# Kernel optimization log

Hardware: AMD Instinct MI355X
Metric: run time of the kernel (lower is better)

Reference implementation:

```python
import jax, jax.numpy as jnp
import numpy as np

R = 10000   # relation_num
E = 256     # emb_size == hidden_size
B = 1024    # batch
L = 8       # body length (loop runs L-1 steps)


def setup_inputs() -> dict:
    key = jax.random.key(0)
    ks = jax.random.split(key, 10)
    s = 0.05
    return {
        "bodys": jax.random.randint(ks[0], (B, L), 0, R),
        "emb_w": jax.random.normal(ks[1], (R, E), jnp.float32) * s,
        "w_ih": jax.random.normal(ks[2], (4 * E, E), jnp.float32) * s,
        "w_hh": jax.random.normal(ks[3], (4 * E, E), jnp.float32) * s,
        "b_ih": jax.random.normal(ks[4], (4 * E,), jnp.float32) * s,
        "b_hh": jax.random.normal(ks[5], (4 * E,), jnp.float32) * s,
        "fc1_w": jax.random.normal(ks[6], (E, 2 * E), jnp.float32) * s,
        "fc1_b": jax.random.normal(ks[7], (E,), jnp.float32) * s,
        "fc2_w": jax.random.normal(ks[8], (R + 1, E), jnp.float32) * s,
        "fc2_b": jax.random.normal(ks[9], (R + 1,), jnp.float32) * s,
    }


def _lstm(x, w_ih, w_hh, b_ih, b_hh):
    # x: [B, L, E] -> hidden states [B, L, H] (torch gate order i,f,g,o)
    Bn, _, H = x.shape[0], x.shape[1], w_hh.shape[1]
    h0 = jnp.zeros((Bn, H), x.dtype)
    c0 = jnp.zeros((Bn, H), x.dtype)

    def step(carry, xt):
        h, c = carry
        g = xt @ w_ih.T + b_ih + h @ w_hh.T + b_hh
        i, f, gg, o = jnp.split(g, 4, axis=-1)
        c = jax.nn.sigmoid(f) * c + jax.nn.sigmoid(i) * jnp.tanh(gg)
        h = jax.nn.sigmoid(o) * jnp.tanh(c)
        return (h, c), h

    _, hs = jax.lax.scan(step, (h0, c0), x.transpose(1, 0, 2))
    return hs.transpose(1, 0, 2)


def reference(bodys, emb_w, w_ih, w_hh, b_ih, b_hh, fc1_w, fc1_b, fc2_w, fc2_b):
    x = emb_w[bodys]                       # [B, L, E] embedded body relations
    body_hid = _lstm(x, w_ih, w_hh, b_ih, b_hh)  # [B, L, E]
    Rn = emb_w.shape[0]
    prob = emb_concat = prob_sf = None
    for i in range(body_hid.shape[1] - 1):   # short fixed unroll (L-1 steps)
        if i == 0:
            emb_1 = x[:, 0, :]
            second = x[:, 1, :]
        else:
            # prob_sf @ cat(embedding(indices), body_hid[:, i])  without [B,R+1,E]
            emb_1 = prob_sf[:, :Rn] @ emb_w + prob_sf[:, Rn:] * body_hid[:, i, :]
            # relation_emb[:, i+1, :] == emb_w[i+1] broadcast over batch
            second = jnp.broadcast_to(emb_w[i + 1], emb_1.shape)
        emb_concat = jnp.concatenate([emb_1, second], axis=1)   # [B, 2E]
        prob = jax.nn.relu(emb_concat @ fc1_w.T + fc1_b) @ fc2_w.T + fc2_b  # [B, R+1]
        prob_sf = jax.nn.softmax(prob, axis=1)
    return prob, emb_concat
```

## Files before the change

### kernel.cpp

```cpp
#include <hip/hip_runtime.h>

#define Bv 1024
#define Ev 256
#define Lv 8
#define Rv 10000
#define NP1 10001
#define PS2 10240
#define NPAD 10112
#define BM 64
#define BN 128
#define BK 32
#define NSLICE 16
#define NSLOT 158
#define RPSTRIDE 160

typedef __attribute__((ext_vector_type(8))) short bf16x8;
typedef __attribute__((ext_vector_type(4))) float f32x4;

__device__ __forceinline__ float b2f(unsigned short u) {
    union { unsigned int i; float f; } v; v.i = ((unsigned int)u) << 16; return v.f;
}
__device__ __forceinline__ unsigned short f2b(float f) {
    union { float f; unsigned int i; } v; v.f = f;
    unsigned int r = v.i + 0x7fffu + ((v.i >> 16) & 1u);
    return (unsigned short)(r >> 16);
}
__device__ __forceinline__ void glds16(const void* g, void* l) {
    __builtin_amdgcn_global_load_lds(
        (const __attribute__((address_space(1))) void*)g,
        (__attribute__((address_space(3))) void*)l, 16, 0, 0);
}

__global__ __launch_bounds__(256) void gemm_tile(
    const unsigned short* __restrict__ A1, int lda1,
    const unsigned short* __restrict__ W1, int ldw1,
    const float* __restrict__ bias1,
    int Ktot, int kchunk, int Ncols, int mode,
    float* __restrict__ outF, unsigned short* __restrict__ outB, int ldc,
    float* __restrict__ rowPart, float* __restrict__ sfLastU)
{
    __shared__ unsigned short As[BM * BK];
    __shared__ unsigned short Bs[BN * BK];

    int bmode = mode & 7;
    int swz   = mode >> 4;
    int bx, by, bz;
    if (swz == 1) {
        int r = blockIdx.x & 7, q = blockIdx.x >> 3;
        bx = q & 15; by = r + (q >> 4) * 8; bz = 0;
        if (by >= NPAD / BN) return;
    } else if (swz == 2) {
        int r = blockIdx.x & 7, q = blockIdx.x >> 3;
        bz = r + (q >> 5) * 8; bx = (q & 31) >> 1; by = q & 1;
    } else {
        bx = blockIdx.x; by = blockIdx.y; bz = blockIdx.z;
    }

    int tid  = threadIdx.x;
    int wave = tid >> 6;
    int lane = tid & 63;
    int quad = lane >> 4;
    int l16  = lane & 15;
    int wm = (wave & 1) * 32;
    int wn = (wave >> 1) * 64;
    int m0 = bx * BM;
    int n0 = by * BN;
    int k0 = bz * kchunk;
    int k1 = k0 + kchunk; if (k1 > Ktot) k1 = Ktot;

    f32x4 acc[2][4];
#pragma unroll
    for (int i = 0; i < 2; ++i)
#pragma unroll
        for (int j = 0; j < 4; ++j) acc[i][j] = (f32x4){0.f, 0.f, 0.f, 0.f};

    int c0 = tid, c1 = 256 + tid;
    int row0 = c0 >> 2, row1 = c1 >> 2;
    int g80 = ((c0 & 3) ^ (row0 & 3) ^ ((row0 >> 2) & 3)) * 8;
    int g81 = ((c1 & 3) ^ (row1 & 3) ^ ((row1 >> 2) & 3)) * 8;
    unsigned short* ldsA0 = As + (size_t)(wave * 64) * 8;
    unsigned short* ldsB0 = Bs + (size_t)(wave * 64) * 8;
    unsigned short* ldsB1 = Bs + (size_t)(256 + wave * 64) * 8;

    bool first = true;
    for (int k = k0; k < k1; k += BK) {
        if (!first) __syncthreads();
        first = false;
        glds16(A1 + (size_t)(m0 + row0) * lda1 + k + g80, ldsA0);
        glds16(W1 + (size_t)(n0 + row0) * ldw1 + k + g80, ldsB0);
        glds16(W1 + (size_t)(n0 + row1) * ldw1 + k + g81, ldsB1);
        asm volatile("s_waitcnt vmcnt(0)" ::: "memory");
        __syncthreads();

        bf16x8 af[2], bfr[4];
#pragma unroll
        for (int t = 0; t < 2; ++t) {
            int m = wm + t * 16 + l16;
            int ca = quad ^ (m & 3) ^ ((m >> 2) & 3);
            af[t] = *(const bf16x8*)(As + m * 32 + ca * 8);
        }
#pragma unroll
        for (int t = 0; t < 4; ++t) {
            int n = wn + t * 16 + l16;
            int cb = quad ^ (n & 3) ^ ((n >> 2) & 3);
            bfr[t] = *(const bf16x8*)(Bs + n * 32 + cb * 8);
        }
#pragma unroll
        for (int i = 0; i < 2; ++i)
#pragma unroll
            for (int j = 0; j < 4; ++j)
                acc[i][j] = __builtin_amdgcn_mfma_f32_16x16x32_bf16(
                    af[i], bfr[j], acc[i][j], 0, 0, 0);
    }

    if (bmode == 5) {
        float rsum[2][4];
#pragma unroll
        for (int i = 0; i < 2; ++i)
#pragma unroll
            for (int r = 0; r < 4; ++r) rsum[i][r] = 0.f;
#pragma unroll
        for (int j = 0; j < 4; ++j) {
            int n = n0 + wn + j * 16 + l16;
            bool valid = (n < Ncols);
            float bsum = valid ? bias1[n] : 0.f;
#pragma unroll
            for (int i = 0; i < 2; ++i) {
                int mBase = m0 + wm + i * 16 + quad * 4;
#pragma unroll
                for (int r = 0; r < 4; ++r) {
                    float e = 0.f;
                    unsigned short w = 0;
                    if (valid) {
                        e = expf(acc[i][j][r] + bsum);
                        w = f2b(e);
                        if (n == Rv) sfLastU[mBase + r] = e;
                    }
                    outB[(size_t)(mBase + r) * ldc + n] = w;
                    rsum[i][r] += e;
                }
            }
        }
        int slot = by * 2 + (wn >> 6);
#pragma unroll
        for (int i = 0; i < 2; ++i)
#pragma unroll
            for (int r = 0; r < 4; ++r) {
                float s = rsum[i][r];
                s += __shfl_xor(s, 1);
                s += __shfl_xor(s, 2);
                s += __shfl_xor(s, 4);
                s += __shfl_xor(s, 8);
                if (l16 == 0) {
                    int m = m0 + wm + i * 16 + quad * 4 + r;
                    rowPart[(size_t)m * RPSTRIDE + slot] = s;
                }
            }
        return;
    }

#pragma unroll
    for (int j = 0; j < 4; ++j) {
        int n = n0 + wn + j * 16 + l16;
        if (n >= Ncols) continue;
        float bsum = bias1 ? bias1[n] : 0.f;
#pragma unroll
        for (int i = 0; i < 2; ++i) {
            int mBase = m0 + wm + i * 16 + quad * 4;
#pragma unroll
            for (int r = 0; r < 4; ++r) {
                float v = acc[i][j][r] + bsum;
                size_t idx = (size_t)(mBase + r) * ldc + n;
                if (bmode == 0)      outF[idx] = v;
                else                 outF[(size_t)bz * (Bv * Ev) + idx] = v;
            }
        }
    }
}

__global__ __launch_bounds__(256) void gemm64(
    const unsigned short* __restrict__ A1, int lda1,
    const unsigned short* __restrict__ W1, int ldw1,
    const unsigned short* __restrict__ A2, int lda2,
    const unsigned short* __restrict__ W2, int ldw2,
    const float* __restrict__ bias1,
    int Ktot, int Ncols, int mode,
    float* __restrict__ outF, unsigned short* __restrict__ outB,
    int ldc, int nshift)
{
    __shared__ unsigned short As[64 * 32];
    __shared__ unsigned short Bs[64 * 32];

    int bmode = mode & 7;
    int bx = blockIdx.x >> nshift;
    int by = blockIdx.x & ((1 << nshift) - 1);
    int tid  = threadIdx.x;
    int wave = tid >> 6;
    int lane = tid & 63;
    int quad = lane >> 4;
    int l16  = lane & 15;
    int m0 = bx * 64;
    int n0 = by * 64;

    f32x4 acc[4];
#pragma unroll
    for (int j = 0; j < 4; ++j) acc[j] = (f32x4){0.f, 0.f, 0.f, 0.f};

    int row = tid >> 2;
    int g8  = ((tid & 3) ^ (row & 3) ^ ((row >> 2) & 3)) * 8;
    unsigned short* ldsA = As + wave * 512;
    unsigned short* ldsB = Bs + wave * 512;

    int nSrc = A2 ? 2 : 1;
    bool first = true;
    for (int s = 0; s < nSrc; ++s) {
        const unsigned short* A = s ? A2 : A1; int lda = s ? lda2 : lda1;
        const unsigned short* W = s ? W2 : W1; int ldw = s ? ldw2 : ldw1;
        for (int k = 0; k < Ktot; k += 32) {
            if (!first) __syncthreads();
            first = false;
            glds16(A + (size_t)(m0 + row) * lda + k + g8, ldsA);
            glds16(W + (size_t)(n0 + row) * ldw + k + g8, ldsB);
            asm volatile("s_waitcnt vmcnt(0)" ::: "memory");
            __syncthreads();

            int ml = wave * 16 + l16;
            int ca = quad ^ (ml & 3) ^ ((ml >> 2) & 3);
            bf16x8 a = *(const bf16x8*)(As + ml * 32 + ca * 8);
#pragma unroll
            for (int j = 0; j < 4; ++j) {
                int nl = j * 16 + l16;
                int cb = quad ^ (nl & 3) ^ ((nl >> 2) & 3);
                bf16x8 b = *(const bf16x8*)(Bs + nl * 32 + cb * 8);
                acc[j] = __builtin_amdgcn_mfma_f32_16x16x32_bf16(a, b, acc[j], 0, 0, 0);
            }
        }
    }

    if (bmode == 4) {
        int e  = by * 16 + l16;
        float bi = bias1[n0 + l16];
        float bf_ = bias1[n0 + 16 + l16];
        float bg = bias1[n0 + 32 + l16];
        float bo = bias1[n0 + 48 + l16];
#pragma unroll
        for (int r = 0; r < 4; ++r) {
            int m = m0 + wave * 16 + quad * 4 + r;
            float gi = acc[0][r] + bi;
            float gf = acc[1][r] + bf_;
            float gg = acc[2][r] + bg;
            float go = acc[3][r] + bo;
            float cp = (mode & 8) ? 0.f : outF[(size_t)m * 256 + e];
            float si = 1.f / (1.f + expf(-gi));
            float sf = 1.f / (1.f + expf(-gf));
            float so = 1.f / (1.f + expf(-go));
            float cn = sf * cp + si * tanhf(gg);
            outF[(size_t)m * 256 + e] = cn;
            outB[(size_t)m * 256 + e] = f2b(so * tanhf(cn));
        }
        return;
    }

#pragma unroll
    for (int j = 0; j < 4; ++j) {
        int n = n0 + j * 16 + l16;
        if (n >= Ncols) continue;
        float bsum = bias1 ? bias1[n] : 0.f;
#pragma unroll
        for (int r = 0; r < 4; ++r) {
            int m = m0 + wave * 16 + quad * 4 + r;
            float v = acc[j][r] + bsum;
            if (bmode == 1) outB[(size_t)m * ldc + n] = f2b(v > 0.f ? v : 0.f);
            else            outB[(size_t)m * ldc + n] = f2b(v);
        }
    }
}

__global__ void prep_k(const float* __restrict__ w_ih,
                       const float* __restrict__ w_hh,
                       const float* __restrict__ fc1_w,
                       const float* __restrict__ fc2_w,
                       const float* __restrict__ b_ih,
                       const float* __restrict__ b_hh,
                       const int* __restrict__ bodys,
                       const float* __restrict__ emb_w,
                       unsigned short* __restrict__ w_ih_b,
                       unsigned short* __restrict__ w_hh_b,
                       unsigned short* __restrict__ fc1_w_b,
                       unsigned short* __restrict__ fc2_w_b,
                       float* __restrict__ biasC,
                       unsigned short* __restrict__ x)
{
    int b = blockIdx.x, t = threadIdx.x;
    if (b < 1264) {
#pragma unroll
        for (int j = 0; j < 8; ++j) {
            int i = b * 2048 + j * 256 + t;
            fc2_w_b[i] = (i < NP1 * Ev) ? f2b(fc2_w[i]) : (unsigned short)0;
        }
    } else if (b < 1520) {
        int bb = b - 1264;
        const float* src = (bb < 128) ? w_ih : w_hh;
        unsigned short* dst = (bb < 128) ? w_ih_b : w_hh_b;
        int rb = (bb & 127) * 8;
#pragma unroll
        for (int j = 0; j < 8; ++j) {
            int r = rb + j;
            int gate = (r >> 4) & 3;
            int e = (r & 15) | ((r >> 6) << 4);
            dst[(size_t)r * 256 + t] = f2b(src[(size_t)(gate * 256 + e) * 256 + t]);
        }
    } else if (b < 1584) {
        int base = (b - 1520) * 2048;
#pragma unroll
        for (int j = 0; j < 8; ++j) {
            int i = base + j * 256 + t;
            fc1_w_b[i] = f2b(fc1_w[i]);
        }
    } else if (b < 1585) {
#pragma unroll
        for (int j = 0; j < 4; ++j) {
            int r = j * 256 + t;
            int gate = (r >> 4) & 3;
            int e = (r & 15) | ((r >> 6) << 4);
            biasC[r] = b_ih[gate * 256 + e] + b_hh[gate * 256 + e];
        }
    } else {
        int bb = b - 1585;
#pragma unroll
        for (int j = 0; j < 8; ++j) {
            int row = bb * 8 + j;
            x[(size_t)row * Ev + t] = f2b(emb_w[(size_t)bodys[row] * Ev + t]);
        }
    }
}

__global__ void transpose_emb(const float* __restrict__ emb_w,
                              unsigned short* __restrict__ embT)
{
    __shared__ float tile[32][33];
    int kt = blockIdx.x * 32, et = blockIdx.y * 32;
    int tx = threadIdx.x & 31, ty = threadIdx.x >> 5;
#pragma unroll
    for (int r = ty; r < 32; r += 8) {
        int k = kt + r;
        tile[r][tx] = (k < Rv) ? emb_w[(size_t)k * Ev + et + tx] : 0.f;
    }
    __syncthreads();
#pragma unroll
    for (int r = ty; r < 32; r += 8) {
        embT[(size_t)(et + r) * PS2 + kt + tx] = f2b(tile[tx][r]);
    }
}

__global__ void concat0(const int* __restrict__ bodys,
                        const float* __restrict__ emb_w,
                        unsigned short* __restrict__ embc,
                        unsigned short* __restrict__ sfA)
{
    int b = blockIdx.x, e = threadIdx.x;
    embc[(size_t)b * 512 + e]       = f2b(emb_w[(size_t)bodys[b * Lv + 0] * Ev + e]);
    embc[(size_t)b * 512 + 256 + e] = f2b(emb_w[(size_t)bodys[b * Lv + 1] * Ev + e]);
    if (e < PS2 - NPAD) sfA[(size_t)b * PS2 + NPAD + e] = 0;
}

__global__ void finalize_emb(const float* __restrict__ emb1p,
                             const float* __restrict__ rowPart,
                             const float* __restrict__ sfLastU,
                             const unsigned short* __restrict__ h_i,
                             const float* __restrict__ emb_row,
                             unsigned short* __restrict__ embc,
                             float* __restrict__ outTail)
{
    int b = blockIdx.x, e = threadIdx.x;
    int wave = e >> 6, lane = e & 63;
    __shared__ float sred[4];
    float ps = (e < NSLOT) ? rowPart[(size_t)b * RPSTRIDE + e] : 0.f;
    for (int off = 32; off; off >>= 1) ps += __shfl_down(ps, off);
    if (lane == 0) sred[wave] = ps;
    __syncthreads();
    float inv = 1.f / (sred[0] + sred[1] + sred[2] + sred[3]);

    float v = 0.f;
#pragma unroll
    for (int z = 0; z < NSLICE; ++z)
        v += emb1p[(size_t)z * (Bv * Ev) + (size_t)b * Ev + e];
    v += sfLastU[b] * b2f(h_i[(size_t)b * Ev + e]);
    v *= inv;
    float w = emb_row[e];
    embc[(size_t)b * 512 + e]       = f2b(v);
    embc[(size_t)b * 512 + 256 + e] = f2b(w);
    if (outTail) {
        outTail[(size_t)b * 512 + e]       = v;
        outTail[(size_t)b * 512 + 256 + e] = w;
    }
}

extern "C" void kernel_launch(void* const* d_in, const int* in_sizes, int n_in,
                              void* d_out, int out_size, void* d_ws, size_t ws_size,
                              hipStream_t stream)
{
    const int*   bodys = (const int*)d_in[0];
    const float* emb_w = (const float*)d_in[1];
    const float* w_ih  = (const float*)d_in[2];
    const float* w_hh  = (const float*)d_in[3];
    const float* b_ih  = (const float*)d_in[4];
    const float* b_hh  = (const float*)d_in[5];
    const float* fc1_w = (const float*)d_in[6];
    const float* fc1_b = (const float*)d_in[7];
    const float* fc2_w = (const float*)d_in[8];
    const float* fc2_b = (const float*)d_in[9];
    float* out = (float*)d_out;

    char* ws = (char*)d_ws;
    size_t off = 0;
    auto alloc = [&](size_t bytes) -> void* {
        void* p = ws + off;
        off += (bytes + 255) & ~(size_t)255;
        return p;
    };
    unsigned short* x       = (unsigned short*)alloc((size_t)Bv * Lv * Ev * 2);
    unsigned short* hs      = (unsigned short*)alloc((size_t)Lv * Bv * Ev * 2);
    float*          cbuf    = (float*)alloc((size_t)Bv * Ev * 4);
    unsigned short* embT    = (unsigned short*)alloc((size_t)Ev * PS2 * 2);
    unsigned short* sfA     = (unsigned short*)alloc((size_t)Bv * PS2 * 2);
    float*          sfLastU = (float*)alloc((size_t)Bv * 4);
    float*          rowPart = (float*)alloc((size_t)Bv * RPSTRIDE * 4);
    float*          emb1p   = (float*)alloc((size_t)NSLICE * Bv * Ev * 4);
    unsigned short* embc    = (unsigned short*)alloc((size_t)Bv * 512 * 2);
    unsigned short* hiddenA = (unsigned short*)alloc((size_t)Bv * Ev * 2);
    unsigned short* w_ih_b  = (unsigned short*)alloc((size_t)1024 * Ev * 2);
    unsigned short* w_hh_b  = (unsigned short*)alloc((size_t)1024 * Ev * 2);
    float*          biasC   = (float*)alloc((size_t)1024 * 4);
    unsigned short* fc1_w_b = (unsigned short*)alloc((size_t)Ev * 512 * 2);
    unsigned short* fc2_w_b = (unsigned short*)alloc((size_t)NPAD * Ev * 2);
    (void)ws_size; (void)in_sizes; (void)n_in; (void)out_size;

    prep_k<<<2609, 256, 0, stream>>>(w_ih, w_hh, fc1_w, fc2_w, b_ih, b_hh,
                                     bodys, emb_w,
                                     w_ih_b, w_hh_b, fc1_w_b, fc2_w_b, biasC, x);
    transpose_emb<<<dim3(PS2 / 32, Ev / 32), 256, 0, stream>>>(emb_w, embT);

    for (int t = 0; t < Lv; ++t) {
        gemm64<<<256, 256, 0, stream>>>(
            x + t * Ev, Lv * Ev, w_ih_b, Ev,
            (t == 0) ? nullptr : (hs + (size_t)(t - 1) * Bv * Ev), Ev, w_hh_b, Ev,
            biasC,
            Ev, 1024, 4 | (t == 0 ? 8 : 0),
            cbuf, hs + (size_t)t * Bv * Ev, 1024, 4);
    }

    for (int i = 0; i < 7; ++i) {
        if (i == 0) {
            concat0<<<Bv, 256, 0, stream>>>(bodys, emb_w, embc, sfA);
        } else {
            gemm_tile<<<512, 256, 0, stream>>>(
                sfA, PS2, embT, PS2,
                nullptr,
                PS2, PS2 / NSLICE, Ev, 2 | (2 << 4),
                emb1p, nullptr, Ev, nullptr, nullptr);
            finalize_emb<<<Bv, 256, 0, stream>>>(
                emb1p, rowPart, sfLastU, hs + (size_t)i * Bv * Ev,
                emb_w + (size_t)(i + 1) * Ev, embc,
                (i == 6) ? (out + (size_t)Bv * NP1) : nullptr);
        }
        gemm64<<<64, 256, 0, stream>>>(
            embc, 512, fc1_w_b, 512, nullptr, 0, nullptr, 0,
            fc1_b,
            512, 256, 1,
            nullptr, hiddenA, 256, 2);
        if (i < 6) {
            gemm_tile<<<1280, 256, 0, stream>>>(
                hiddenA, Ev, fc2_w_b, Ev,
                fc2_b,
                Ev, Ev, NP1, 5 | (1 << 4),
                nullptr, sfA, PS2, rowPart, sfLastU);
        } else {
            gemm_tile<<<1280, 256, 0, stream>>>(
                hiddenA, Ev, fc2_w_b, Ev,
                fc2_b,
                Ev, Ev, NP1, 0 | (1 << 4),
                out, nullptr, NP1, nullptr, nullptr);
        }
    }
}
```

Before: 499.1 us.

## Load GEMM fragments directly from global memory, dropping LDS staging and barriers

Both GEMM kernels now read their MFMA operand fragments straight from global memory into registers instead of staging tiles through shared memory with global_load_lds and two barriers per K step. The loop is unrolled by two so the compiler can overlap loads with MFMAs. This removes the sync and LDS traffic, but the tiles are no longer shared: each wave re-fetches A and W rows that other waves also need, which shifts more load onto L1/L2 and uses strided 16-byte row accesses.

After: 750.0 us. +50.3%, slower.

```diff
diff --git a/kernel.cpp b/kernel.cpp
--- a/kernel.cpp
+++ b/kernel.cpp
@@ -25,11 +25,6 @@
     unsigned int r = v.i + 0x7fffu + ((v.i >> 16) & 1u);
     return (unsigned short)(r >> 16);
 }
-__device__ __forceinline__ void glds16(const void* g, void* l) {
-    __builtin_amdgcn_global_load_lds(
-        (const __attribute__((address_space(1))) void*)g,
-        (__attribute__((address_space(3))) void*)l, 16, 0, 0);
-}
 
 __global__ __launch_bounds__(256) void gemm_tile(
     const unsigned short* __restrict__ A1, int lda1,
@@ -39,9 +34,6 @@
     float* __restrict__ outF, unsigned short* __restrict__ outB, int ldc,
     float* __restrict__ rowPart, float* __restrict__ sfLastU)
 {
-    __shared__ unsigned short As[BM * BK];
-    __shared__ unsigned short Bs[BN * BK];
-
     int bmode = mode & 7;
     int swz   = mode >> 4;
     int bx, by, bz;
@@ -74,37 +66,22 @@
 #pragma unroll
         for (int j = 0; j < 4; ++j) acc[i][j] = (f32x4){0.f, 0.f, 0.f, 0.f};
 
-    int c0 = tid, c1 = 256 + tid;
-    int row0 = c0 >> 2, row1 = c1 >> 2;
-    int g80 = ((c0 & 3) ^ (row0 & 3) ^ ((row0 >> 2) & 3)) * 8;
-    int g81 = ((c1 & 3) ^ (row1 & 3) ^ ((row1 >> 2) & 3)) * 8;
-    unsigned short* ldsA0 = As + (size_t)(wave * 64) * 8;
-    unsigned short* ldsB0 = Bs + (size_t)(wave * 64) * 8;
-    unsigned short* ldsB1 = Bs + (size_t)(256 + wave * 64) * 8;
-
-    bool first = true;
+    const unsigned short* Ar0 = A1 + (size_t)(m0 + wm + l16) * lda1 + quad * 8;
+    const unsigned short* Ar1 = Ar0 + (size_t)16 * lda1;
+    const unsigned short* Wr0 = W1 + (size_t)(n0 + wn + l16) * ldw1 + quad * 8;
+    const unsigned short* Wr1 = Wr0 + (size_t)16 * ldw1;
+    const unsigned short* Wr2 = Wr0 + (size_t)32 * ldw1;
+    const unsigned short* Wr3 = Wr0 + (size_t)48 * ldw1;
+
+#pragma unroll 2
     for (int k = k0; k < k1; k += BK) {
-        if (!first) __syncthreads();
-        first = false;
-        glds16(A1 + (size_t)(m0 + row0) * lda1 + k + g80, ldsA0);
-        glds16(W1 + (size_t)(n0 + row0) * ldw1 + k + g80, ldsB0);
-        glds16(W1 + (size_t)(n0 + row1) * ldw1 + k + g81, ldsB1);
-        asm volatile("s_waitcnt vmcnt(0)" ::: "memory");
-        __syncthreads();
-
         bf16x8 af[2], bfr[4];
-#pragma unroll
-        for (int t = 0; t < 2; ++t) {
-            int m = wm + t * 16 + l16;
-            int ca = quad ^ (m & 3) ^ ((m >> 2) & 3);
-            af[t] = *(const bf16x8*)(As + m * 32 + ca * 8);
-        }
-#pragma unroll
-        for (int t = 0; t < 4; ++t) {
-            int n = wn + t * 16 + l16;
-            int cb = quad ^ (n & 3) ^ ((n >> 2) & 3);
-            bfr[t] = *(const bf16x8*)(Bs + n * 32 + cb * 8);
-        }
+        af[0]  = *(const bf16x8*)(Ar0 + k);
+        af[1]  = *(const bf16x8*)(Ar1 + k);
+        bfr[0] = *(const bf16x8*)(Wr0 + k);
+        bfr[1] = *(const bf16x8*)(Wr1 + k);
+        bfr[2] = *(const bf16x8*)(Wr2 + k);
+        bfr[3] = *(const bf16x8*)(Wr3 + k);
 #pragma unroll
         for (int i = 0; i < 2; ++i)
 #pragma unroll
@@ -188,9 +165,6 @@
     float* __restrict__ outF, unsigned short* __restrict__ outB,
     int ldc, int nshift)
 {
-    __shared__ unsigned short As[64 * 32];
-    __shared__ unsigned short Bs[64 * 32];
-
     int bmode = mode & 7;
     int bx = blockIdx.x >> nshift;
     int by = blockIdx.x & ((1 << nshift) - 1);
@@ -206,34 +180,28 @@
 #pragma unroll
     for (int j = 0; j < 4; ++j) acc[j] = (f32x4){0.f, 0.f, 0.f, 0.f};
 
-    int row = tid >> 2;
-    int g8  = ((tid & 3) ^ (row & 3) ^ ((row >> 2) & 3)) * 8;
-    unsigned short* ldsA = As + wave * 512;
-    unsigned short* ldsB = Bs + wave * 512;
+    int ml = m0 + wave * 16 + l16;
 
     int nSrc = A2 ? 2 : 1;
-    bool first = true;
     for (int s = 0; s < nSrc; ++s) {
         const unsigned short* A = s ? A2 : A1; int lda = s ? lda2 : lda1;
         const unsigned short* W = s ? W2 : W1; int ldw = s ? ldw2 : ldw1;
+        const unsigned short* Ar  = A + (size_t)ml * lda + quad * 8;
+        const unsigned short* Wr0 = W + (size_t)(n0 + l16) * ldw + quad * 8;
+        const unsigned short* Wr1 = Wr0 + (size_t)16 * ldw;
+        const unsigned short* Wr2 = Wr0 + (size_t)32 * ldw;
+        const unsigned short* Wr3 = Wr0 + (size_t)48 * ldw;
+#pragma unroll 2
         for (int k = 0; k < Ktot; k += 32) {
-            if (!first) __syncthreads();
-            first = false;
-            glds16(A + (size_t)(m0 + row) * lda + k + g8, ldsA);
-            glds16(W + (size_t)(n0 + row) * ldw + k + g8, ldsB);
-            asm volatile("s_waitcnt vmcnt(0)" ::: "memory");
-            __syncthreads();
-
-            int ml = wave * 16 + l16;
-            int ca = quad ^ (ml & 3) ^ ((ml >> 2) & 3);
-            bf16x8 a = *(const bf16x8*)(As + ml * 32 + ca * 8);
-#pragma unroll
-            for (int j = 0; j < 4; ++j) {
-                int nl = j * 16 + l16;
-                int cb = quad ^ (nl & 3) ^ ((nl >> 2) & 3);
-                bf16x8 b = *(const bf16x8*)(Bs + nl * 32 + cb * 8);
-                acc[j] = __builtin_amdgcn_mfma_f32_16x16x32_bf16(a, b, acc[j], 0, 0, 0);
-            }
+            bf16x8 a  = *(const bf16x8*)(Ar + k);
+            bf16x8 b0 = *(const bf16x8*)(Wr0 + k);
+            bf16x8 b1 = *(const bf16x8*)(Wr1 + k);
+            bf16x8 b2 = *(const bf16x8*)(Wr2 + k);
+            bf16x8 b3 = *(const bf16x8*)(Wr3 + k);
+            acc[0] = __builtin_amdgcn_mfma_f32_16x16x32_bf16(a, b0, acc[0], 0, 0, 0);
+            acc[1] = __builtin_amdgcn_mfma_f32_16x16x32_bf16(a, b1, acc[1], 0, 0, 0);
+            acc[2] = __builtin_amdgcn_mfma_f32_16x16x32_bf16(a, b2, acc[2], 0, 0, 0);
+            acc[3] = __builtin_amdgcn_mfma_f32_16x16x32_bf16(a, b3, acc[3], 0, 0, 0);
         }
     }
 
```
